# Kernel optimization log

Measured on AMD Instinct MI355X. Metric: run time of the kernel, lower is better.

Reference implementation:

```python
import jax, jax.numpy as jnp
import numpy as np

NUM_HEAD = 16
EMBED_DIM = 1024
HEAD_DIM = EMBED_DIM // NUM_HEAD
QK_DIM = EMBED_DIM  # qk_dim defaults to embed_dim


def setup_inputs() -> dict:
    key = jax.random.key(0)
    k1, k2, k3 = jax.random.split(key, 3)
    x = jax.random.normal(k1, (4, 2048, EMBED_DIM), dtype=jnp.float32)
    # xavier_uniform-like init scale
    lim_qkv = float(np.sqrt(6.0 / (EMBED_DIM + 3 * EMBED_DIM)))
    lim_out = float(np.sqrt(6.0 / (EMBED_DIM + EMBED_DIM)))
    W_QKV = jax.random.uniform(k2, (EMBED_DIM, 3 * EMBED_DIM), jnp.float32, -lim_qkv, lim_qkv)
    W_Out = jax.random.uniform(k3, (EMBED_DIM, EMBED_DIM), jnp.float32, -lim_out, lim_out)
    return {"x": x, "W_QKV": W_QKV, "W_Out": W_Out}


def reference(x, W_QKV, W_Out):
    bsz, slen, _ = x.shape
    # [b,s,3E] -> [b,s,H,hd,3] -> [b,H,s,hd,3]  (interleaved qkv layout, as in torch source)
    qkv = (x @ W_QKV).reshape(bsz, slen, NUM_HEAD, HEAD_DIM, 3).transpose(0, 2, 1, 3, 4)
    q, k, v = qkv[..., 0], qkv[..., 1], qkv[..., 2]
    # NOTE: module scales by sqrt(qk_dim) (full dim), not sqrt(head_dim)
    scores = jnp.einsum("bhqd,bhkd->bhqk", q, k) / np.sqrt(QK_DIM).astype(np.float32)
    attn = jax.nn.softmax(scores, axis=-1)  # dropout p=0.0 -> identity
    out = jnp.einsum("bhqk,bhkd->bhqd", attn, v)  # [b,H,s,hd]
    out = out.transpose(0, 2, 1, 3).reshape(bsz, slen, EMBED_DIM)
    return out @ W_Out
```

## Files before the change

### kernel.cpp

```cpp
#include <hip/hip_runtime.h>
#include <stdint.h>

typedef __bf16 bf16x8 __attribute__((ext_vector_type(8)));
typedef __bf16 bf16x4_t __attribute__((ext_vector_type(4)));
typedef float f32x4 __attribute__((ext_vector_type(4)));
typedef unsigned short u16x8 __attribute__((ext_vector_type(8)));
typedef unsigned short u16x4 __attribute__((ext_vector_type(4)));
typedef short s16x4 __attribute__((ext_vector_type(4)));
typedef unsigned int u32x2 __attribute__((ext_vector_type(2)));

#if __has_builtin(__builtin_amdgcn_exp2f)
#define EXP2(x) __builtin_amdgcn_exp2f(x)
#else
#define EXP2(x) exp2f(x)
#endif

#if __has_builtin(__builtin_amdgcn_s_setprio)
#define SETPRIO(n) __builtin_amdgcn_s_setprio(n)
#else
#define SETPRIO(n)
#endif

__device__ __forceinline__ unsigned short f2bf(float f) {
    unsigned int u = __float_as_uint(f);
    u += 0x7fffu + ((u >> 16) & 1u);
    return (unsigned short)(u >> 16);
}

__device__ __forceinline__ int swz64(int row, int c) {
    return (c & 7) | ((((c >> 3) ^ row) & 7) << 3);
}

__device__ __forceinline__ int vperm64(int d, int s) {
    int chunk = ((s >> 5) << 2) + ((s >> 2) & 3);
    return (((s >> 4) & 1) << 2) + (s & 3) + (((chunk ^ d) & 7) << 3);
}

__device__ __forceinline__ void glds16(const unsigned short* g, unsigned short* l) {
    __builtin_amdgcn_global_load_lds((const __attribute__((address_space(1))) void*)g,
                                     (__attribute__((address_space(3))) void*)l, 16, 0, 0);
}

__device__ __forceinline__ void transpose_body(const float* __restrict__ in,
                                               unsigned short* __restrict__ out,
                                               unsigned short (*tile)[33],
                                               int K, int N, int permute, int nb, int kb) {
    int tx = threadIdx.x & 31, ty = threadIdx.x >> 5;
    #pragma unroll
    for (int r = ty; r < 32; r += 8)
        tile[r][tx] = f2bf(in[(size_t)(kb + r) * N + nb + tx]);
    __syncthreads();
    #pragma unroll
    for (int r = ty; r < 32; r += 8) {
        int n_orig = nb + r, col = kb + tx;
        int row;
        if (permute) {
            int h = n_orig / 192, rem = n_orig - h * 192;
            int d = rem / 3, cc = rem - 3 * d;
            row = cc * 1024 + h * 64 + d;
        } else {
            row = n_orig;
        }
        out[(size_t)row * K + (col & ~63) + swz64(row, col & 63)] = tile[tx][r];
    }
}

__global__ __launch_bounds__(256) void preprocess_kernel(const float* __restrict__ x,
                                                         const float* __restrict__ wqkv,
                                                         const float* __restrict__ wout,
                                                         unsigned short* __restrict__ xb,
                                                         unsigned short* __restrict__ wqkvt,
                                                         unsigned short* __restrict__ woutt) {
    __shared__ unsigned short tile[32][33];
    int bid = blockIdx.x;
    if (bid < 4096) {
        size_t id = (size_t)bid * 256 + threadIdx.x;
        int row = (int)(id >> 7);
        int cid = (int)(id & 127);
        const float4* src = (const float4*)(x + id * 8);
        float4 a = src[0], b = src[1];
        u16x8 o;
        o[0] = f2bf(a.x); o[1] = f2bf(a.y); o[2] = f2bf(a.z); o[3] = f2bf(a.w);
        o[4] = f2bf(b.x); o[5] = f2bf(b.y); o[6] = f2bf(b.z); o[7] = f2bf(b.w);
        int group = cid >> 3, ch = cid & 7;
        *(u16x8*)(xb + (size_t)row * 1024 + group * 64 + (((ch ^ row) & 7) << 3)) = o;
    } else if (bid < 7168) {
        int idx = bid - 4096;
        transpose_body(wqkv, wqkvt, tile, 1024, 3072, 1, (idx % 96) * 32, (idx / 96) * 32);
    } else {
        int idx = bid - 7168;
        transpose_body(wout, woutt, tile, 1024, 1024, 0, (idx % 32) * 32, (idx / 32) * 32);
    }
}

__device__ __forceinline__ void gemm128_mainloop(const unsigned short* __restrict__ A,
                                                 const unsigned short* __restrict__ Bt,
                                                 f32x4 acc[4][4]) {
    __shared__ unsigned short smem[4 * 128 * 64];
    const int t = threadIdx.x, lane = t & 63, w = t >> 6;
    const int wm = w & 1, wn = w >> 1;
    const int r16 = lane & 15, quad = lane >> 4;
    const size_t mb = (size_t)blockIdx.y * 128, nb = (size_t)blockIdx.x * 128;

    const f32x4 zf = {0.f, 0.f, 0.f, 0.f};
    #pragma unroll
    for (int i = 0; i < 4; i++)
        #pragma unroll
        for (int j = 0; j < 4; j++) acc[i][j] = zf;

    int aoff[2], boff[2];
    #pragma unroll
    for (int kkh = 0; kkh < 2; kkh++) {
        int chunk = ((kkh * 4 + quad) ^ (r16 & 7)) << 3;
        aoff[kkh] = (wm * 64 + r16) * 64 + chunk;
        boff[kkh] = (wn * 64 + r16) * 64 + chunk;
    }

    const unsigned short* ap = A + (mb + w * 32 + (lane >> 3)) * 1024 + (lane & 7) * 8;
    const unsigned short* bp = Bt + (nb + w * 32 + (lane >> 3)) * 1024 + (lane & 7) * 8;
    unsigned short* al = smem + w * 2048;
    unsigned short* bl = smem + 16384 + w * 2048;
    auto stage = [&](int reg) {
        #pragma unroll
        for (int c = 0; c < 4; c++) {
            glds16(ap + c * 8192, al + reg * 8192 + c * 512);
            glds16(bp + c * 8192, bl + reg * 8192 + c * 512);
        }
        ap += 64;
        bp += 64;
    };

    auto body = [&](const unsigned short* as, const unsigned short* bs) {
        #pragma unroll
        for (int kkh = 0; kkh < 2; kkh++) {
            bf16x8 af[4], bfv[4];
            #pragma unroll
            for (int i = 0; i < 4; i++) af[i] = *(const bf16x8*)(as + i * 1024 + aoff[kkh]);
            #pragma unroll
            for (int j = 0; j < 4; j++) bfv[j] = *(const bf16x8*)(bs + j * 1024 + boff[kkh]);
            SETPRIO(1);
            #pragma unroll
            for (int i = 0; i < 4; i++)
                #pragma unroll
                for (int j = 0; j < 4; j++)
                    acc[i][j] =
                        __builtin_amdgcn_mfma_f32_16x16x32_bf16(af[i], bfv[j], acc[i][j], 0, 0, 0);
            SETPRIO(0);
        }
    };

    const unsigned short* A0 = smem;
    const unsigned short* A1 = smem + 8192;
    const unsigned short* B0 = smem + 16384;
    const unsigned short* B1 = smem + 24576;

    stage(0);
    #pragma unroll 1
    for (int j = 0; j < 7; j++) {
        __syncthreads();
        stage(1);
        body(A0, B0);
        __syncthreads();
        stage(0);
        body(A1, B1);
    }
    __syncthreads();
    stage(1);
    body(A0, B0);
    __syncthreads();
    body(A1, B1);
}

__global__ __launch_bounds__(256) void gemm_qkv_kernel(const unsigned short* __restrict__ A,
                                                       const unsigned short* __restrict__ Bt,
                                                       unsigned short* __restrict__ Qo,
                                                       unsigned short* __restrict__ Ko,
                                                       unsigned short* __restrict__ Vo) {
    f32x4 acc[4][4];
    gemm128_mainloop(A, Bt, acc);
    const int t = threadIdx.x, lane = t & 63, w = t >> 6;
    const int wm = w & 1, wn = w >> 1;
    const int c16 = lane & 15, quad = lane >> 4;
    const int mb = blockIdx.y * 128, nb = blockIdx.x * 128;
    const int cls = nb >> 10;
    const int hh = ((nb & 1023) >> 6) + wn;
    const float SCALE_Q = 1.4426950408889634f / 32.0f;
    #pragma unroll
    for (int i = 0; i < 4; i++) {
        #pragma unroll
        for (int r = 0; r < 4; r++) {
            int m = mb + wm * 64 + i * 16 + quad * 4 + r;
            int b = m >> 11, s = m & 2047;
            int bh = b * 16 + hh;
            #pragma unroll
            for (int j = 0; j < 4; j++) {
                int d = j * 16 + c16;
                float v = acc[i][j][r];
                if (cls == 0)
                    Qo[((size_t)bh * 2048 + s) * 64 + swz64(s, d)] = f2bf(v * SCALE_Q);
                else if (cls == 1)
                    Ko[((size_t)bh * 2048 + s) * 64 + swz64(s, d)] = f2bf(v);
                else
                    Vo[((size_t)bh * 64 + d) * 2048 + (s & ~63) + vperm64(d, s & 63)] = f2bf(v);
            }
        }
    }
}

__global__ __launch_bounds__(256) void gemm_out_kernel(const unsigned short* __restrict__ A,
                                                       const unsigned short* __restrict__ Bt,
                                                       float* __restrict__ C) {
    f32x4 acc[4][4];
    gemm128_mainloop(A, Bt, acc);
    const int t = threadIdx.x, lane = t & 63, w = t >> 6;
    const int wm = w & 1, wn = w >> 1;
    const int c16 = lane & 15, quad = lane >> 4;
    const int mb = blockIdx.y * 128, nb = blockIdx.x * 128;
    #pragma unroll
    for (int i = 0; i < 4; i++)
        #pragma unroll
        for (int j = 0; j < 4; j++)
            #pragma unroll
            for (int r = 0; r < 4; r++) {
                int m = mb + wm * 64 + i * 16 + quad * 4 + r;
                int n = nb + wn * 64 + j * 16 + c16;
                C[(size_t)m * 1024 + n] = acc[i][j][r];
            }
}

__global__ __launch_bounds__(256) void attn_kernel(const unsigned short* __restrict__ Qg,
                                                   const unsigned short* __restrict__ Kg,
                                                   const unsigned short* __restrict__ Vt,
                                                   unsigned short* __restrict__ O) {
    __shared__ unsigned short smem[4 * 64 * 64];
    unsigned short* K0 = smem;
    unsigned short* K1 = smem + 4096;
    unsigned short* V0 = smem + 8192;
    unsigned short* V1 = smem + 12288;
    const int t = threadIdx.x, lane = t & 63, w = t >> 6;
    const int c16 = lane & 15, quad = lane >> 4;
    const int bh = blockIdx.y, q0 = blockIdx.x * 128;

    bf16x8 qf[2][2];
    #pragma unroll
    for (int qt = 0; qt < 2; qt++) {
        int row = q0 + w * 32 + qt * 16 + c16;
        #pragma unroll
        for (int kkh = 0; kkh < 2; kkh++) {
            int c = kkh * 32 + quad * 8;
            qf[qt][kkh] = *(const bf16x8*)(Qg + ((size_t)bh * 2048 + row) * 64 + swz64(row, c));
        }
    }

    int coff[2];
    #pragma unroll
    for (int h = 0; h < 2; h++)
        coff[h] = c16 * 64 + ((((h * 4 + quad) ^ c16) & 7) << 3);

    const unsigned short* kgp =
        Kg + ((size_t)bh * 2048 + w * 16 + (lane >> 3)) * 64 + (lane & 7) * 8;
    const unsigned short* vgp =
        Vt + ((size_t)bh * 64 + w * 16 + (lane >> 3)) * 2048 + (lane & 7) * 8;
    unsigned short* kl = smem + (w * 16) * 64;
    auto stage = [&](int reg) {
        #pragma unroll
        for (int c = 0; c < 2; c++) {
            glds16(kgp + c * 512, kl + reg * 4096 + c * 512);
            glds16(vgp + c * 16384, kl + 8192 + reg * 4096 + c * 512);
        }
        kgp += 4096;
        vgp += 64;
    };

    const f32x4 zf = {0.f, 0.f, 0.f, 0.f};
    f32x4 acc_o[2][4];
    float den[2] = {0.f, 0.f};
    #pragma unroll
    for (int qt = 0; qt < 2; qt++)
        #pragma unroll
        for (int dt = 0; dt < 4; dt++) acc_o[qt][dt] = zf;

    auto body = [&](const unsigned short* ks, const unsigned short* vs) {
        f32x4 sacc[4][2];
        {
            bf16x8 kf[4];
            #pragma unroll
            for (int kt = 0; kt < 4; kt++)
                kf[kt] = *(const bf16x8*)(ks + kt * 1024 + coff[0]);
            SETPRIO(1);
            #pragma unroll
            for (int kt = 0; kt < 4; kt++)
                #pragma unroll
                for (int qt = 0; qt < 2; qt++)
                    sacc[kt][qt] =
                        __builtin_amdgcn_mfma_f32_16x16x32_bf16(kf[kt], qf[qt][0], zf, 0, 0, 0);
            SETPRIO(0);
        }
        {
            bf16x8 kf[4];
            #pragma unroll
            for (int kt = 0; kt < 4; kt++)
                kf[kt] = *(const bf16x8*)(ks + kt * 1024 + coff[1]);
            SETPRIO(1);
            #pragma unroll
            for (int kt = 0; kt < 4; kt++)
                #pragma unroll
                for (int qt = 0; qt < 2; qt++)
                    sacc[kt][qt] = __builtin_amdgcn_mfma_f32_16x16x32_bf16(kf[kt], qf[qt][1],
                                                                           sacc[kt][qt], 0, 0, 0);
            SETPRIO(0);
        }
        #pragma unroll
        for (int g = 0; g < 2; g++) {
            bf16x8 vf[4];
            #pragma unroll
            for (int dt = 0; dt < 4; dt++)
                vf[dt] = *(const bf16x8*)(vs + dt * 1024 + coff[g]);
            #pragma unroll
            for (int qt = 0; qt < 2; qt++) {
                float e0 = EXP2(sacc[2 * g][qt][0]);
                float e1 = EXP2(sacc[2 * g][qt][1]);
                float e2 = EXP2(sacc[2 * g][qt][2]);
                float e3 = EXP2(sacc[2 * g][qt][3]);
                float e4 = EXP2(sacc[2 * g + 1][qt][0]);
                float e5 = EXP2(sacc[2 * g + 1][qt][1]);
                float e6 = EXP2(sacc[2 * g + 1][qt][2]);
                float e7 = EXP2(sacc[2 * g + 1][qt][3]);
                den[qt] += ((e0 + e1) + (e2 + e3)) + ((e4 + e5) + (e6 + e7));
                bf16x8 pb = {(__bf16)e0, (__bf16)e1, (__bf16)e2, (__bf16)e3,
                             (__bf16)e4, (__bf16)e5, (__bf16)e6, (__bf16)e7};
                SETPRIO(1);
                #pragma unroll
                for (int dt = 0; dt < 4; dt++)
                    acc_o[qt][dt] =
                        __builtin_amdgcn_mfma_f32_16x16x32_bf16(pb, vf[dt], acc_o[qt][dt], 0, 0, 0);
                SETPRIO(0);
            }
        }
    };

    stage(0);
    #pragma unroll 1
    for (int it2 = 0; it2 < 15; it2++) {
        __syncthreads();
        stage(1);
        body(K0, V0);
        __syncthreads();
        stage(0);
        body(K1, V1);
    }
    __syncthreads();
    stage(1);
    body(K0, V0);
    __syncthreads();
    body(K1, V1);

    #pragma unroll
    for (int qt = 0; qt < 2; qt++) {
        den[qt] += __shfl_xor(den[qt], 16);
        den[qt] += __shfl_xor(den[qt], 32);
    }

    const int b = bh >> 4, h = bh & 15;
    #pragma unroll
    for (int qt = 0; qt < 2; qt++) {
        #pragma unroll
        for (int r = 0; r < 4; r++) {
            float rd = 1.0f / __shfl(den[qt], quad * 4 + r);
            int srow = q0 + w * 32 + qt * 16 + quad * 4 + r;
            #pragma unroll
            for (int dt = 0; dt < 4; dt++) {
                int col = dt * 16 + c16;
                O[((size_t)b * 2048 + srow) * 1024 + h * 64 + swz64(srow, col)] =
                    f2bf(acc_o[qt][dt][r] * rd);
            }
        }
    }
}

extern "C" void kernel_launch(void* const* d_in, const int* in_sizes, int n_in,
                              void* d_out, int out_size, void* d_ws, size_t ws_size,
                              hipStream_t stream) {
    (void)in_sizes; (void)n_in; (void)out_size; (void)ws_size;
    const float* x = (const float*)d_in[0];
    const float* wqkv = (const float*)d_in[1];
    const float* wout = (const float*)d_in[2];
    float* out = (float*)d_out;

    const size_t SZ_X = 8388608;
    const size_t SZ_WQKV = 3145728;
    const size_t SZ_WOUT = 1048576;

    unsigned short* ws = (unsigned short*)d_ws;
    unsigned short* xb = ws;
    unsigned short* wqkvt = xb + SZ_X;
    unsigned short* woutt = wqkvt + SZ_WQKV;
    unsigned short* Qa = woutt + SZ_WOUT;
    unsigned short* Ka = Qa + SZ_X;
    unsigned short* Va = Ka + SZ_X;
    unsigned short* attn = Va + SZ_X;

    preprocess_kernel<<<8192, 256, 0, stream>>>(x, wqkv, wout, xb, wqkvt, woutt);
    gemm_qkv_kernel<<<dim3(24, 64), 256, 0, stream>>>(xb, wqkvt, Qa, Ka, Va);
    attn_kernel<<<dim3(16, 64), 256, 0, stream>>>(Qa, Ka, Va, attn);
    gemm_out_kernel<<<dim3(8, 64), 256, 0, stream>>>(attn, woutt, out);
}
```

Measured before the change: 283.0 us.

## Switch attention kernel to 32x32x16 MFMA tiles with remapped V layout

```diff
diff --git a/kernel.cpp b/kernel.cpp
--- a/kernel.cpp
+++ b/kernel.cpp
@@ -2,12 +2,15 @@
 #include <stdint.h>
 
 typedef __bf16 bf16x8 __attribute__((ext_vector_type(8)));
-typedef __bf16 bf16x4_t __attribute__((ext_vector_type(4)));
 typedef float f32x4 __attribute__((ext_vector_type(4)));
+typedef float f32x16 __attribute__((ext_vector_type(16)));
 typedef unsigned short u16x8 __attribute__((ext_vector_type(8)));
-typedef unsigned short u16x4 __attribute__((ext_vector_type(4)));
-typedef short s16x4 __attribute__((ext_vector_type(4)));
-typedef unsigned int u32x2 __attribute__((ext_vector_type(2)));
+
+#if __has_builtin(__builtin_amdgcn_mfma_f32_32x32x16_bf16)
+#define MFMA32(a, b, c) __builtin_amdgcn_mfma_f32_32x32x16_bf16((a), (b), (c), 0, 0, 0)
+#else
+static __device__ __forceinline__ f32x16 MFMA32(bf16x8, bf16x8, f32x16 c) { return c; }
+#endif
 
 #if __has_builtin(__builtin_amdgcn_exp2f)
 #define EXP2(x) __builtin_amdgcn_exp2f(x)
@@ -31,9 +34,10 @@
     return (c & 7) | ((((c >> 3) ^ row) & 7) << 3);
 }
 
-__device__ __forceinline__ int vperm64(int d, int s) {
-    int chunk = ((s >> 5) << 2) + ((s >> 2) & 3);
-    return (((s >> 4) & 1) << 2) + (s & 3) + (((chunk ^ d) & 7) << 3);
+__device__ __forceinline__ int vperm32(int d, int s) {
+    int c8 = ((s >> 5) << 2) | (((s >> 4) & 1) << 1) | ((s >> 2) & 1);
+    int intra = (s & 3) | (((s >> 3) & 1) << 2);
+    return intra + (((c8 ^ d) & 7) << 3);
 }
 
 __device__ __forceinline__ void glds16(const unsigned short* g, unsigned short* l) {
@@ -201,7 +205,7 @@
                 else if (cls == 1)
                     Ko[((size_t)bh * 2048 + s) * 64 + swz64(s, d)] = f2bf(v);
                 else
-                    Vo[((size_t)bh * 64 + d) * 2048 + (s & ~63) + vperm64(d, s & 63)] = f2bf(v);
+                    Vo[((size_t)bh * 64 + d) * 2048 + (s & ~63) + vperm32(d, s & 63)] = f2bf(v);
             }
         }
     }
@@ -238,24 +242,24 @@
     unsigned short* V0 = smem + 8192;
     unsigned short* V1 = smem + 12288;
     const int t = threadIdx.x, lane = t & 63, w = t >> 6;
-    const int c16 = lane & 15, quad = lane >> 4;
-    const int bh = blockIdx.y, q0 = blockIdx.x * 128;
-
-    bf16x8 qf[2][2];
-    #pragma unroll
-    for (int qt = 0; qt < 2; qt++) {
-        int row = q0 + w * 32 + qt * 16 + c16;
-        #pragma unroll
-        for (int kkh = 0; kkh < 2; kkh++) {
-            int c = kkh * 32 + quad * 8;
-            qf[qt][kkh] = *(const bf16x8*)(Qg + ((size_t)bh * 2048 + row) * 64 + swz64(row, c));
-        }
-    }
-
-    int coff[2];
-    #pragma unroll
-    for (int h = 0; h < 2; h++)
-        coff[h] = c16 * 64 + ((((h * 4 + quad) ^ c16) & 7) << 3);
+    const int l31 = lane & 31, h = lane >> 5;
+    const int i_disp = blockIdx.y * 16 + blockIdx.x;
+    const int bh = (i_disp & 7) + 8 * (i_disp >> 7);
+    const int q0 = ((i_disp >> 3) & 15) * 128;
+
+    int coff[4];
+    #pragma unroll
+    for (int i = 0; i < 4; i++)
+        coff[i] = l31 * 64 + ((((2 * i + h) ^ l31) & 7) << 3);
+
+    bf16x8 qf[4];
+    {
+        int row = q0 + w * 32 + l31;
+        const unsigned short* qbase = Qg + ((size_t)bh * 2048 + row) * 64;
+        #pragma unroll
+        for (int step = 0; step < 4; step++)
+            qf[step] = *(const bf16x8*)(qbase + ((((2 * step + h) ^ row) & 7) << 3));
+    }
 
     const unsigned short* kgp =
         Kg + ((size_t)bh * 2048 + w * 16 + (lane >> 3)) * 64 + (lane & 7) * 8;
@@ -272,71 +276,55 @@
         vgp += 64;
     };
 
-    const f32x4 zf = {0.f, 0.f, 0.f, 0.f};
-    f32x4 acc_o[2][4];
-    float den[2] = {0.f, 0.f};
-    #pragma unroll
-    for (int qt = 0; qt < 2; qt++)
-        #pragma unroll
-        for (int dt = 0; dt < 4; dt++) acc_o[qt][dt] = zf;
+    const f32x16 z16 = {0.f, 0.f, 0.f, 0.f, 0.f, 0.f, 0.f, 0.f,
+                        0.f, 0.f, 0.f, 0.f, 0.f, 0.f, 0.f, 0.f};
+    f32x16 acc0 = z16, acc1 = z16;
+    float den = 0.f;
+
+    auto pv32 = [&](const f32x16& sg, const unsigned short* vs, int c0) {
+        #pragma unroll
+        for (int p = 0; p < 2; p++) {
+            float e0 = EXP2(sg[8 * p + 0]);
+            float e1 = EXP2(sg[8 * p + 1]);
+            float e2 = EXP2(sg[8 * p + 2]);
+            float e3 = EXP2(sg[8 * p + 3]);
+            float e4 = EXP2(sg[8 * p + 4]);
+            float e5 = EXP2(sg[8 * p + 5]);
+            float e6 = EXP2(sg[8 * p + 6]);
+            float e7 = EXP2(sg[8 * p + 7]);
+            den += ((e0 + e1) + (e2 + e3)) + ((e4 + e5) + (e6 + e7));
+            bf16x8 pb = {(__bf16)e0, (__bf16)e1, (__bf16)e2, (__bf16)e3,
+                         (__bf16)e4, (__bf16)e5, (__bf16)e6, (__bf16)e7};
+            bf16x8 vf0 = *(const bf16x8*)(vs + coff[c0 + p]);
+            bf16x8 vf1 = *(const bf16x8*)(vs + 2048 + coff[c0 + p]);
+            SETPRIO(1);
+            acc0 = MFMA32(pb, vf0, acc0);
+            acc1 = MFMA32(pb, vf1, acc1);
+            SETPRIO(0);
+        }
+    };
 
     auto body = [&](const unsigned short* ks, const unsigned short* vs) {
-        f32x4 sacc[4][2];
+        f32x16 s0, s1;
         {
-            bf16x8 kf[4];
-            #pragma unroll
-            for (int kt = 0; kt < 4; kt++)
-                kf[kt] = *(const bf16x8*)(ks + kt * 1024 + coff[0]);
+            bf16x8 ka = *(const bf16x8*)(ks + coff[0]);
+            bf16x8 kb = *(const bf16x8*)(ks + 2048 + coff[0]);
             SETPRIO(1);
-            #pragma unroll
-            for (int kt = 0; kt < 4; kt++)
-                #pragma unroll
-                for (int qt = 0; qt < 2; qt++)
-                    sacc[kt][qt] =
-                        __builtin_amdgcn_mfma_f32_16x16x32_bf16(kf[kt], qf[qt][0], zf, 0, 0, 0);
+            s0 = MFMA32(ka, qf[0], z16);
+            s1 = MFMA32(kb, qf[0], z16);
             SETPRIO(0);
         }
-        {
-            bf16x8 kf[4];
-            #pragma unroll
-            for (int kt = 0; kt < 4; kt++)
-                kf[kt] = *(const bf16x8*)(ks + kt * 1024 + coff[1]);
+        #pragma unroll
+        for (int step = 1; step < 4; step++) {
+            bf16x8 ka = *(const bf16x8*)(ks + coff[step]);
+            bf16x8 kb = *(const bf16x8*)(ks + 2048 + coff[step]);
             SETPRIO(1);
-            #pragma unroll
-            for (int kt = 0; kt < 4; kt++)
-                #pragma unroll
-                for (int qt = 0; qt < 2; qt++)
-                    sacc[kt][qt] = __builtin_amdgcn_mfma_f32_16x16x32_bf16(kf[kt], qf[qt][1],
-                                                                           sacc[kt][qt], 0, 0, 0);
+            s0 = MFMA32(ka, qf[step], s0);
+            s1 = MFMA32(kb, qf[step], s1);
             SETPRIO(0);
         }
-        #pragma unroll
-        for (int g = 0; g < 2; g++) {
-            bf16x8 vf[4];
-            #pragma unroll
-            for (int dt = 0; dt < 4; dt++)
-                vf[dt] = *(const bf16x8*)(vs + dt * 1024 + coff[g]);
-            #pragma unroll
-            for (int qt = 0; qt < 2; qt++) {
-                float e0 = EXP2(sacc[2 * g][qt][0]);
-                float e1 = EXP2(sacc[2 * g][qt][1]);
-                float e2 = EXP2(sacc[2 * g][qt][2]);
-                float e3 = EXP2(sacc[2 * g][qt][3]);
-                float e4 = EXP2(sacc[2 * g + 1][qt][0]);
-                float e5 = EXP2(sacc[2 * g + 1][qt][1]);
-                float e6 = EXP2(sacc[2 * g + 1][qt][2]);
-                float e7 = EXP2(sacc[2 * g + 1][qt][3]);
-                den[qt] += ((e0 + e1) + (e2 + e3)) + ((e4 + e5) + (e6 + e7));
-                bf16x8 pb = {(__bf16)e0, (__bf16)e1, (__bf16)e2, (__bf16)e3,
-                             (__bf16)e4, (__bf16)e5, (__bf16)e6, (__bf16)e7};
-                SETPRIO(1);
-                #pragma unroll
-                for (int dt = 0; dt < 4; dt++)
-                    acc_o[qt][dt] =
-                        __builtin_amdgcn_mfma_f32_16x16x32_bf16(pb, vf[dt], acc_o[qt][dt], 0, 0, 0);
-                SETPRIO(0);
-            }
-        }
+        pv32(s0, vs, 0);
+        pv32(s1, vs, 2);
     };
 
     stage(0);
@@ -355,26 +343,17 @@
     __syncthreads();
     body(K1, V1);
 
-    #pragma unroll
-    for (int qt = 0; qt < 2; qt++) {
-        den[qt] += __shfl_xor(den[qt], 16);
-        den[qt] += __shfl_xor(den[qt], 32);
-    }
-
-    const int b = bh >> 4, h = bh & 15;
-    #pragma unroll
-    for (int qt = 0; qt < 2; qt++) {
-        #pragma unroll
-        for (int r = 0; r < 4; r++) {
-            float rd = 1.0f / __shfl(den[qt], quad * 4 + r);
-            int srow = q0 + w * 32 + qt * 16 + quad * 4 + r;
-            #pragma unroll
-            for (int dt = 0; dt < 4; dt++) {
-                int col = dt * 16 + c16;
-                O[((size_t)b * 2048 + srow) * 1024 + h * 64 + swz64(srow, col)] =
-                    f2bf(acc_o[qt][dt][r] * rd);
-            }
-        }
+    den += __shfl_xor(den, 32);
+
+    const int b = bh >> 4, hd = bh & 15;
+    #pragma unroll
+    for (int reg = 0; reg < 16; reg++) {
+        int qrl = (reg & 3) + 8 * (reg >> 2) + 4 * h;
+        float rd = 1.0f / __shfl(den, qrl);
+        int srow = q0 + w * 32 + qrl;
+        size_t base = ((size_t)b * 2048 + srow) * 1024 + hd * 64;
+        O[base + swz64(srow, l31)] = f2bf(acc0[reg] * rd);
+        O[base + swz64(srow, 32 + l31)] = f2bf(acc1[reg] * rd);
     }
 }
 
```

Result: faster. 270.0 us (-4.6%).
